# Optimization experiments

Hardware: AMD Instinct MI355X
Metric: run time of the kernel (lower is better)

The kernel has to match this reference:

```python
import jax, jax.numpy as jnp
import numpy as np

B, T, NX = 2, 2048, 512
H = 2                    # n_head (structurally forced to 2 by rns() broadcasting)
L = 64                   # num landmarks (cfg.MODEL.LANDMARK)
K = 32                   # rns neighbors per token
HD = NX // H // 2        # differential head dim = 128
EPS = 1e-5


def setup_inputs() -> dict:
    key = jax.random.key(0)
    ks = jax.random.split(key, 16)
    inp = {}
    inp["x"] = jax.random.normal(ks[0], (B, T, NX), jnp.float32)
    # linear weights (torch nn.Linear stores [out,in], applies x @ W.T)
    inp["wq"] = jax.random.normal(ks[1], (NX, NX), jnp.float32) * 0.02
    inp["wk"] = jax.random.normal(ks[2], (NX, NX), jnp.float32) * 0.02
    inp["wv"] = jax.random.normal(ks[3], (NX, NX), jnp.float32) * 0.02
    inp["wo"] = jax.random.normal(ks[4], (NX, NX), jnp.float32) * 0.02
    # landmark modulation params (kaiming-normal-ish init)
    inp["m1"] = jax.random.normal(ks[5], (2 * H, L, 1), jnp.float32)
    inp["m2"] = jax.random.normal(ks[6], (2 * H, 1, L), jnp.float32)
    # differential-attention lambda params
    inp["lq1"] = jax.random.normal(ks[7], (HD,), jnp.float32) * 0.1
    inp["lk1"] = jax.random.normal(ks[8], (HD,), jnp.float32) * 0.1
    inp["lq2"] = jax.random.normal(ks[9], (HD,), jnp.float32) * 0.1
    inp["lk2"] = jax.random.normal(ks[10], (HD,), jnp.float32) * 0.1
    inp["rms_g"] = jnp.ones((2 * HD,), jnp.float32)
    inp["l"] = 3  # layer depth for lambda_init_fn
    inp["num_landmark"] = L
    inp["rns_indices"] = jax.random.randint(ks[11], (B, T, K), 0, T)
    # random.sample(range(t), L) -> distinct indices
    inp["landmark"] = jax.random.permutation(ks[12], T)[:L]
    return inp


def _forward(x, wq, wk, wv, wo, m1, m2, lq1, lk1, lq2, lk2, rms_g,
             l, rns_indices, landmark):
    b, t, nx = x.shape
    hd = nx // H // 2
    q = x @ wq.T
    k = x @ wk.T
    v = x @ wv.T
    qh = q.reshape(b, t, 2 * H, hd).transpose(0, 2, 1, 3)   # [b,2H,t,hd]
    kh = k.reshape(b, t, 2 * H, hd).transpose(0, 2, 3, 1)   # [b,2H,hd,t]
    vh = v.reshape(b, t, H, 2 * hd).transpose(0, 2, 1, 3)   # [b,H,t,2hd]

    # landmark (Nystrom) low-rank factors, L2-normalized over head dim
    sq = qh[:, :, landmark, :]                               # [b,2H,L,hd]
    sk = kh[:, :, :, landmark]                               # [b,2H,hd,L]
    sq = sq / jnp.linalg.norm(sq, axis=3, keepdims=True)
    sk = sk / jnp.linalg.norm(sk, axis=2, keepdims=True)
    sq = m1[None] * sq
    sk = m2[None] * sk

    w1 = jnp.matmul(qh, sk)                                  # [b,2H,t,L]
    w2 = jnp.matmul(sq, kh)                                  # [b,2H,L,t]
    w = jnp.matmul(w1, w2)                                   # [b,2H,t,t]

    lam_init = 0.8 - 0.6 * np.exp(-0.3 * l)
    lam = jnp.exp(jnp.sum(lq1 * lk1)) - jnp.exp(jnp.sum(lq2 * lk2)) + lam_init

    # rns symmetric sparse mask: mask[b,i,j]=1 iff j in rns_indices[b,i] AND i in rns_indices[b,j]
    bi = jnp.arange(b)[:, None, None]
    ti = jnp.arange(t)[None, :, None]
    m = jnp.zeros((b, t, t), x.dtype).at[bi, ti, rns_indices].set(1.0)
    m = m * m.transpose(0, 2, 1)
    m4 = m[:, None]                                          # broadcast over heads

    p = jax.nn.softmax(w * m4 - 1e9 * (1.0 - m4), axis=-1)   # [b,2H,t,t]
    p5 = p.reshape(b, H, 2, t, t)
    # differential mixing (note: second term indexes the HEAD dim, requires H==2)
    wmix = (p5[:, :, 0] - lam * p5[:, :, 1]) + ((1.0 - lam) * p5[:, 1] - p5[:, 0])
    a = jnp.matmul(wmix, vh)                                 # [b,H,t,2hd]

    # RMSNorm sub-layer + (1 - lambda_init) scaling
    a = a * jax.lax.rsqrt(jnp.mean(a * a, axis=-1, keepdims=True) + EPS) * rms_g
    a = a * (1.0 - lam_init)
    return a.transpose(0, 2, 1, 3).reshape(b, t, H * 2 * hd) @ wo.T


def reference(x, wq, wk, wv, wo, m1, m2, lq1, lk1, lq2, lk2, rms_g,
              l, num_landmark, rns_indices, landmark):
    return _forward(x, wq, wk, wv, wo, m1, m2, lq1, lk1, lq2, lk2, rms_g,
                    l, rns_indices, landmark)
```

## Files before the change

### kernel.cpp

```cpp
#include <hip/hip_runtime.h>
#include <hip/hip_bf16.h>

#define BB 2
#define TT 2048
#define NX 512
#define NH 4
#define HD 128
#define LL 64
#define KK 32

typedef __bf16 bf16x8 __attribute__((ext_vector_type(8)));
typedef float f32x4 __attribute__((ext_vector_type(4)));
typedef unsigned short us;
typedef const unsigned int __attribute__((address_space(1)))* gptr_t;
typedef unsigned int __attribute__((address_space(3)))* lptr_t;

__device__ __forceinline__ us f2bf(float f) {
    unsigned u = __float_as_uint(f);
    unsigned r = (u + 0x7fffu + ((u >> 16) & 1u)) >> 16;
    return (us)r;
}
__device__ __forceinline__ float bf2f(us h) {
    return __uint_as_float(((unsigned)h) << 16);
}

__global__ void k_split_all(const float* __restrict__ x,
                            const float* __restrict__ wq, const float* __restrict__ wk,
                            const float* __restrict__ wv, const float* __restrict__ wo,
                            us* __restrict__ x_hi, us* __restrict__ x_lo,
                            us* __restrict__ wqkv_hi, us* __restrict__ wqkv_lo,
                            us* __restrict__ wo_hi, us* __restrict__ wo_lo,
                            const float* __restrict__ lq1, const float* __restrict__ lk1,
                            const float* __restrict__ lq2, const float* __restrict__ lk2,
                            const int* __restrict__ lint, float* __restrict__ scal,
                            float* __restrict__ cs)
{
    const int bidx = blockIdx.x;
    if (bidx == 3072) {
        const int tid = threadIdx.x;
        const f32x4 z = {0.f, 0.f, 0.f, 0.f};
        *reinterpret_cast<f32x4*>(cs + tid * 4) = z;
        if (tid < 64) {
            float s1 = lq1[tid] * lk1[tid] + lq1[tid + 64] * lk1[tid + 64];
            float s2 = lq2[tid] * lk2[tid] + lq2[tid + 64] * lk2[tid + 64];
            for (int off = 32; off; off >>= 1) { s1 += __shfl_xor(s1, off); s2 += __shfl_xor(s2, off); }
            if (tid == 0) {
                float lam_init = 0.8f - 0.6f * expf(-0.3f * (float)lint[0]);
                scal[0] = expf(s1) - expf(s2) + lam_init;
                scal[1] = lam_init;
            }
        }
        return;
    }
    const float* src;
    us* hi;
    us* lo;
    int pos;
    if (bidx < 2048) {
        src = x; hi = x_hi; lo = x_lo;
        pos = bidx * 1024 + threadIdx.x * 4;
    } else {
        const int w = (bidx - 2048) >> 8;
        const int p = (bidx - 2048) & 255;
        pos = p * 1024 + threadIdx.x * 4;
        if (w == 0)      { src = wq; hi = wqkv_hi;          lo = wqkv_lo; }
        else if (w == 1) { src = wk; hi = wqkv_hi + 262144; lo = wqkv_lo + 262144; }
        else if (w == 2) { src = wv; hi = wqkv_hi + 524288; lo = wqkv_lo + 524288; }
        else             { src = wo; hi = wo_hi;            lo = wo_lo; }
    }
    const float4 v = *reinterpret_cast<const float4*>(src + pos);
    ushort4 h, l;
    h.x = f2bf(v.x); l.x = f2bf(v.x - bf2f(h.x));
    h.y = f2bf(v.y); l.y = f2bf(v.y - bf2f(h.y));
    h.z = f2bf(v.z); l.z = f2bf(v.z - bf2f(h.z));
    h.w = f2bf(v.w); l.w = f2bf(v.w - bf2f(h.w));
    *reinterpret_cast<ushort4*>(hi + pos) = h;
    *reinterpret_cast<ushort4*>(lo + pos) = l;
}

template<int BN, int MODE>
__global__ __launch_bounds__(256) void k_gemm_big(
    const us* __restrict__ a_hi, const us* __restrict__ a_lo,
    const us* __restrict__ b_hi, const us* __restrict__ b_lo,
    us* __restrict__ vb, float* __restrict__ cout,
    us* __restrict__ qs_hi, us* __restrict__ qs_lo,
    us* __restrict__ ks_hi, us* __restrict__ ks_lo)
{
    constexpr int NB = BN / 32;
    __shared__ us lsA[64 * 64];
    __shared__ us lsB[BN * 64];
    const int tid = threadIdx.x;
    const int m0 = blockIdx.x * 64, n0 = blockIdx.y * BN;
    const int region = n0 >> 9;
    const int ncol0 = n0 & 511;
    const int l = tid & 63, wid = tid >> 6;
    const int wr = (wid >> 1) * 32, wc = (wid & 1) * (BN / 2);
    const int lr = l & 15;
    const int lkb = (l >> 4) * 16;
    f32x4 acc[2][NB] = {};

    const int r8 = tid >> 3;
    const int swzc8 = (((tid & 7) ^ (r8 & 7)) * 8);

    const int nstep = (MODE == 0) ? (region < 2 ? 24 : 16) : 16;
    for (int kt = 0; kt < nstep; ++kt) {
        const int seg = kt >> 3;
        const int koff = (kt & 7) * 64;
        const us* ab;
        const us* bb;
        if constexpr (MODE == 0) {
            if (region < 2) {
                ab = (seg < 2 ? a_hi : a_lo) + koff + swzc8;
                bb = (seg == 1 ? b_lo : b_hi) + koff + swzc8;
            } else {
                ab = (seg == 0 ? a_hi : a_lo) + koff + swzc8;
                bb = b_hi + koff + swzc8;
            }
        } else {
            ab = (seg == 0 ? a_hi : a_lo) + koff + swzc8;
            bb = b_hi + koff + swzc8;
        }
        #pragma unroll
        for (int j = 0; j < 2; ++j)
            __builtin_amdgcn_global_load_lds((gptr_t)(ab + (size_t)(m0 + j * 32 + r8) * 512),
                                             (lptr_t)(lsA + j * 2048 + tid * 8), 16, 0, 0);
        #pragma unroll
        for (int j = 0; j < BN / 32; ++j)
            __builtin_amdgcn_global_load_lds((gptr_t)(bb + (size_t)(n0 + j * 32 + r8) * 512),
                                             (lptr_t)(lsB + j * 2048 + tid * 8), 16, 0, 0);
        __syncthreads();
        bf16x8 af[2][2], bfr[NB][2];
        #pragma unroll
        for (int m = 0; m < 2; ++m) {
            const int row = wr + m * 16 + lr;
            #pragma unroll
            for (int kk = 0; kk < 2; ++kk) {
                const int cb = (kk * 64 + lkb) ^ ((row & 7) << 4);
                af[m][kk] = *reinterpret_cast<const bf16x8*>(
                    (const char*)lsA + row * 128 + cb);
            }
        }
        #pragma unroll
        for (int n = 0; n < NB; ++n) {
            const int row = wc + n * 16 + lr;
            #pragma unroll
            for (int kk = 0; kk < 2; ++kk) {
                const int cb = (kk * 64 + lkb) ^ ((row & 7) << 4);
                bfr[n][kk] = *reinterpret_cast<const bf16x8*>(
                    (const char*)lsB + row * 128 + cb);
            }
        }
        #pragma unroll
        for (int kk = 0; kk < 2; ++kk)
            #pragma unroll
            for (int m = 0; m < 2; ++m)
                #pragma unroll
                for (int n = 0; n < NB; ++n)
                    acc[m][n] = __builtin_amdgcn_mfma_f32_16x16x32_bf16(
                        af[m][kk], bfr[n][kk], acc[m][n], 0, 0, 0);
        __syncthreads();
    }

    if constexpr (MODE == 0) {
        if (region < 2) {
            us* sh = (region == 0) ? qs_hi : ks_hi;
            us* slo = (region == 0) ? qs_lo : ks_lo;
            #pragma unroll
            for (int m = 0; m < 2; ++m) {
                const int row = m0 + wr + m * 16 + (l >> 4) * 4;
                #pragma unroll
                for (int n = 0; n < NB; ++n) {
                    const int col = ncol0 + wc + n * 16 + lr;
                    #pragma unroll
                    for (int r = 0; r < 4; ++r) {
                        const float val = acc[m][n][r];
                        const us h = f2bf(val);
                        sh[(size_t)(row + r) * 512 + col] = h;
                        slo[(size_t)(row + r) * 512 + col] = f2bf(val - bf2f(h));
                    }
                }
            }
        } else {
            #pragma unroll
            for (int m = 0; m < 2; ++m) {
                const int row = m0 + wr + m * 16 + (l >> 4) * 4;
                #pragma unroll
                for (int n = 0; n < NB; ++n) {
                    const int col = ncol0 + wc + n * 16 + lr;
                    #pragma unroll
                    for (int r = 0; r < 4; ++r)
                        vb[(size_t)(row + r) * 512 + col] = f2bf(acc[m][n][r]);
                }
            }
        }
    } else {
        #pragma unroll
        for (int m = 0; m < 2; ++m) {
            const int row = m0 + wr + m * 16 + (l >> 4) * 4;
            #pragma unroll
            for (int n = 0; n < NB; ++n) {
                const int col = n0 + wc + n * 16 + lr;
                #pragma unroll
                for (int r = 0; r < 4; ++r)
                    cout[(size_t)(row + r) * 512 + col] = acc[m][n][r];
            }
        }
    }
}

__global__ __launch_bounds__(256) void k_gemm_w12(
    const us* __restrict__ q_hi, const us* __restrict__ q_lo,
    const us* __restrict__ k_hi, const us* __restrict__ k_lo,
    const us* __restrict__ kn_hi, const us* __restrict__ kn_lo,
    const us* __restrict__ qn_hi, const us* __restrict__ qn_lo,
    float* __restrict__ w1, float* __restrict__ w2t)
{
    __shared__ us lsA[64 * 32];
    __shared__ us lsB[64 * 32];
    const int tid = threadIdx.x;
    const int m0 = blockIdx.x * 64;
    const int y = blockIdx.y;
    const int hh = y % 3, b = y / 3;
    const int h = hh + 1;
    const int z = blockIdx.z;
    const us* ah = (z ? k_hi : q_hi) + ((size_t)b * 2048) * 512 + h * 128;
    const us* al = (z ? k_lo : q_lo) + ((size_t)b * 2048) * 512 + h * 128;
    const us* bh_p = (z ? qn_hi : kn_hi) + (size_t)(b * 4 + h) * 64 * 128;
    const us* bl_p = (z ? qn_lo : kn_lo) + (size_t)(b * 4 + h) * 64 * 128;
    float* C = (z ? w2t : w1) + (size_t)(b * 3 + hh) * 2048 * 64;

    const int l = tid & 63, wid = tid >> 6;
    const int wr = (wid >> 1) * 32, wc = (wid & 1) * 32;
    const int lr = l & 15, lk8 = (l >> 4) * 8;
    f32x4 acc[2][2] = {};
    const int srow = tid >> 2, scol = (tid & 3) * 8;

    for (int kt = 0; kt < 12; ++kt) {
        const int seg = kt >> 2;
        const int koff = (kt & 3) * 32;
        const us* ab = (seg < 2 ? ah : al) + koff + scol;
        const us* bb = (seg == 1 ? bl_p : bh_p) + koff + scol;
        __builtin_amdgcn_global_load_lds((gptr_t)(ab + (size_t)(m0 + srow) * 512),
                                         (lptr_t)(lsA + tid * 8), 16, 0, 0);
        __builtin_amdgcn_global_load_lds((gptr_t)(bb + (size_t)srow * 128),
                                         (lptr_t)(lsB + tid * 8), 16, 0, 0);
        __syncthreads();
        bf16x8 af[2], bfr[2];
        #pragma unroll
        for (int m = 0; m < 2; ++m)
            af[m] = *reinterpret_cast<const bf16x8*>(&lsA[(wr + m * 16 + lr) * 32 + lk8]);
        #pragma unroll
        for (int n = 0; n < 2; ++n)
            bfr[n] = *reinterpret_cast<const bf16x8*>(&lsB[(wc + n * 16 + lr) * 32 + lk8]);
        #pragma unroll
        for (int m = 0; m < 2; ++m)
            #pragma unroll
            for (int n = 0; n < 2; ++n)
                acc[m][n] = __builtin_amdgcn_mfma_f32_16x16x32_bf16(af[m], bfr[n], acc[m][n], 0, 0, 0);
        __syncthreads();
    }

    #pragma unroll
    for (int m = 0; m < 2; ++m) {
        const int row = m0 + wr + m * 16 + (l >> 4) * 4;
        #pragma unroll
        for (int n = 0; n < 2; ++n) {
            const int col = wc + n * 16 + lr;
            #pragma unroll
            for (int r = 0; r < 4; ++r)
                C[(size_t)(row + r) * 64 + col] = acc[m][n][r];
        }
    }
}

__global__ void k_norm_lm(const us* __restrict__ q_hi, const us* __restrict__ q_lo,
                          const us* __restrict__ k_hi, const us* __restrict__ k_lo,
                          const float* __restrict__ m1, const float* __restrict__ m2,
                          const int* __restrict__ landmark,
                          us* __restrict__ qn_hi, us* __restrict__ qn_lo,
                          us* __restrict__ kn_hi, us* __restrict__ kn_lo)
{
    const int idx = blockIdx.x;
    const int l = idx & 63;
    const int h = (idx >> 6) & 3;
    const int b = idx >> 8;
    const int lm = landmark[l];
    const int d = threadIdx.x;

    const size_t qoff = ((size_t)(b * TT + lm)) * NX + h * HD;
    const float qa = bf2f(q_hi[qoff + d]) + bf2f(q_lo[qoff + d]);
    const float qb = bf2f(q_hi[qoff + d + 64]) + bf2f(q_lo[qoff + d + 64]);
    const float ka = bf2f(k_hi[qoff + d]) + bf2f(k_lo[qoff + d]);
    const float kb = bf2f(k_hi[qoff + d + 64]) + bf2f(k_lo[qoff + d + 64]);
    float sq = qa * qa + qb * qb;
    float sk = ka * ka + kb * kb;
    for (int off = 32; off; off >>= 1) { sq += __shfl_xor(sq, off); sk += __shfl_xor(sk, off); }
    const float invq = rsqrtf(sq) * m1[h * LL + l];
    const float invk = rsqrtf(sk) * m2[h * LL + l];
    const size_t base = (((size_t)(b * NH + h)) * LL + l) * HD;
    const float vq0 = qa * invq, vq1 = qb * invq;
    const float vk0 = ka * invk, vk1 = kb * invk;
    us h0;
    h0 = f2bf(vq0); qn_hi[base + d] = h0;      qn_lo[base + d] = f2bf(vq0 - bf2f(h0));
    h0 = f2bf(vq1); qn_hi[base + d + 64] = h0; qn_lo[base + d + 64] = f2bf(vq1 - bf2f(h0));
    h0 = f2bf(vk0); kn_hi[base + d] = h0;      kn_lo[base + d] = f2bf(vk0 - bf2f(h0));
    h0 = f2bf(vk1); kn_hi[base + d + 64] = h0; kn_lo[base + d + 64] = f2bf(vk1 - bf2f(h0));
}

__global__ void k_colsum(const us* __restrict__ vb, float* __restrict__ cs)
{
    const int tid = threadIdx.x;
    const int c4 = tid * 4;
    const int b = c4 >> 9, c = c4 & 511;
    const int t0 = blockIdx.x * 64;
    const us* p = vb + ((size_t)(b * TT + t0)) * NX + c;
    f32x4 s = {0.f, 0.f, 0.f, 0.f};
    for (int t = 0; t < 64; ++t) {
        const ushort4 u = *reinterpret_cast<const ushort4*>(p + (size_t)t * NX);
        s[0] += bf2f(u.x); s[1] += bf2f(u.y); s[2] += bf2f(u.z); s[3] += bf2f(u.w);
    }
    atomicAdd(&cs[c4 + 0], s[0]);
    atomicAdd(&cs[c4 + 1], s[1]);
    atomicAdd(&cs[c4 + 2], s[2]);
    atomicAdd(&cs[c4 + 3], s[3]);
}

__global__ __launch_bounds__(256) void k_sparse_attn(
    const float* __restrict__ w1, const float* __restrict__ w2t,
    const us* __restrict__ vb, const float* __restrict__ cs,
    const int* __restrict__ rns, const float* __restrict__ rms_g,
    const float* __restrict__ scal,
    us* __restrict__ ao_hi, us* __restrict__ ao_lo)
{
    const int wid = threadIdx.x >> 6;
    const int lane = threadIdx.x & 63;
    const int bi = blockIdx.x * 4 + wid;
    const int b = bi >> 11, i = bi & 2047;

    __shared__ int   sl[4][32];
    __shared__ float plog[4][96];
    __shared__ float wmm[4][2][32];
    __shared__ float w1s[4][3][64];

    const int myidx = lane & 31;
    const int cand = rns[(size_t)bi * KK + myidx];
    int dup = 0;
    #pragma unroll
    for (int kk = 0; kk < 31; ++kk) {
        const int other = __shfl(cand, kk);
        dup |= (kk < myidx) & (other == cand);
    }
    const int* jrow = rns + ((size_t)(b * TT + cand)) * KK + (lane >> 5) * 16;
    int found = 0;
    #pragma unroll
    for (int kk = 0; kk < 16; ++kk) found |= (jrow[kk] == i);
    found |= __shfl_xor(found, 32);
    const int keep = (!dup) && found;
    const unsigned long long mask = __ballot(keep) & 0xffffffffull;
    const int sc = __popcll(mask);
    const int pos = __popcll(mask & ((1ull << myidx) - 1ull));
    if (lane < 32 && keep) sl[wid][pos] = cand;

    const float lam = scal[0], lam_init = scal[1];

    if (sc > 0) {
        #pragma unroll
        for (int r = 0; r < 3; ++r) {
            const int t = r * 64 + lane;
            const int hh = t >> 6, l2 = t & 63;
            w1s[wid][hh][l2] = w1[(((size_t)(b * 3 + hh)) * TT + i) * LL + l2];
        }
        const int ntask = 3 * sc;
        for (int t0 = 0; t0 < ntask; t0 += 8) {
            const int t = t0 + (lane >> 3);
            float part = 0.f;
            if (t < ntask) {
                const int hh = t % 3, ss = t / 3;
                const int j = sl[wid][ss];
                const float* w2row = w2t + (((size_t)(b * 3 + hh)) * TT + j) * LL + (lane & 7) * 8;
                const float* w1p = &w1s[wid][hh][(lane & 7) * 8];
                #pragma unroll
                for (int e = 0; e < 8; ++e) part += w1p[e] * w2row[e];
            }
            part += __shfl_xor(part, 1);
            part += __shfl_xor(part, 2);
            part += __shfl_xor(part, 4);
            if (t < ntask && (lane & 7) == 0) plog[wid][t] = part;
        }
        if (lane < 3) {
            float mx = -1e30f;
            for (int ss = 0; ss < sc; ++ss) mx = fmaxf(mx, plog[wid][ss * 3 + lane]);
            float s = 0.f;
            for (int ss = 0; ss < sc; ++ss) {
                const float e = expf(plog[wid][ss * 3 + lane] - mx);
                plog[wid][ss * 3 + lane] = e;
                s += e;
            }
            const float inv = 1.0f / s;
            for (int ss = 0; ss < sc; ++ss) plog[wid][ss * 3 + lane] *= inv;
        }
        if (lane < sc) {
            const float p1 = plog[wid][lane * 3 + 0];
            const float p2 = plog[wid][lane * 3 + 1];
            const float p3 = plog[wid][lane * 3 + 2];
            wmm[wid][0][lane] = (1.0f - lam) * p2 - lam * p1;
            wmm[wid][1][lane] = p2 - p1 + (1.0f - 2.0f * lam) * p3;
        }
    }

    f32x4 acc0 = {0.f, 0.f, 0.f, 0.f}, acc1 = {0.f, 0.f, 0.f, 0.f};
    if (sc == 0) {
        const float cc = (1.0f - 2.0f * lam) * (1.0f / (float)TT);
        const f32x4 c0 = *reinterpret_cast<const f32x4*>(cs + b * NX + lane * 4);
        const f32x4 c1 = *reinterpret_cast<const f32x4*>(cs + b * NX + 256 + lane * 4);
        acc0 = cc * c0;
        acc1 = cc * c1;
    } else {
        for (int ss = 0; ss < sc; ++ss) {
            const float wa = wmm[wid][0][ss], wb = wmm[wid][1][ss];
            const us* vrow = vb + ((size_t)(b * TT + sl[wid][ss])) * NX;
            const ushort4 ua = *reinterpret_cast<const ushort4*>(vrow + lane * 4);
            const ushort4 ub = *reinterpret_cast<const ushort4*>(vrow + 256 + lane * 4);
            acc0[0] += wa * bf2f(ua.x); acc0[1] += wa * bf2f(ua.y);
            acc0[2] += wa * bf2f(ua.z); acc0[3] += wa * bf2f(ua.w);
            acc1[0] += wb * bf2f(ub.x); acc1[1] += wb * bf2f(ub.y);
            acc1[2] += wb * bf2f(ub.z); acc1[3] += wb * bf2f(ub.w);
        }
    }

    float s0 = acc0[0]*acc0[0] + acc0[1]*acc0[1] + acc0[2]*acc0[2] + acc0[3]*acc0[3];
    float s1 = acc1[0]*acc1[0] + acc1[1]*acc1[1] + acc1[2]*acc1[2] + acc1[3]*acc1[3];
    #pragma unroll
    for (int off = 32; off; off >>= 1) { s0 += __shfl_xor(s0, off); s1 += __shfl_xor(s1, off); }
    const float sc0 = rsqrtf(s0 * (1.0f / 256.0f) + 1e-5f);
    const float sc1 = rsqrtf(s1 * (1.0f / 256.0f) + 1e-5f);
    const float og = 1.0f - lam_init;
    const f32x4 g = *reinterpret_cast<const f32x4*>(rms_g + lane * 4);
    ushort4 h0, l0, h1, l1;
    #pragma unroll
    for (int e = 0; e < 4; ++e) {
        const float v0 = acc0[e] * sc0 * g[e] * og;
        const float v1 = acc1[e] * sc1 * g[e] * og;
        const us a = f2bf(v0);
        const us bq = f2bf(v1);
        (&h0.x)[e] = a;  (&l0.x)[e] = f2bf(v0 - bf2f(a));
        (&h1.x)[e] = bq; (&l1.x)[e] = f2bf(v1 - bf2f(bq));
    }
    *reinterpret_cast<ushort4*>(ao_hi + (size_t)bi * NX + lane * 4) = h0;
    *reinterpret_cast<ushort4*>(ao_lo + (size_t)bi * NX + lane * 4) = l0;
    *reinterpret_cast<ushort4*>(ao_hi + (size_t)bi * NX + 256 + lane * 4) = h1;
    *reinterpret_cast<ushort4*>(ao_lo + (size_t)bi * NX + 256 + lane * 4) = l1;
}

extern "C" void kernel_launch(void* const* d_in, const int* in_sizes, int n_in,
                              void* d_out, int out_size, void* d_ws, size_t ws_size,
                              hipStream_t stream)
{
    const float* x    = (const float*)d_in[0];
    const float* wq   = (const float*)d_in[1];
    const float* wk   = (const float*)d_in[2];
    const float* wv   = (const float*)d_in[3];
    const float* wo   = (const float*)d_in[4];
    const float* m1   = (const float*)d_in[5];
    const float* m2   = (const float*)d_in[6];
    const float* lq1  = (const float*)d_in[7];
    const float* lk1  = (const float*)d_in[8];
    const float* lq2  = (const float*)d_in[9];
    const float* lk2  = (const float*)d_in[10];
    const float* rmsg = (const float*)d_in[11];
    const int*   lint = (const int*)d_in[12];
    const int*   rns  = (const int*)d_in[14];
    const int*   lmk  = (const int*)d_in[15];
    float* out = (float*)d_out;
    float* ws  = (float*)d_ws;

    const size_t M2 = 2097152;
    const size_t W3 = 786432;
    float* w1   = ws;
    float* w2t  = ws + W3;
    float* cs   = ws + 2 * W3;
    float* scal = cs + 1024;
    us* S = (us*)(scal + 128);
    us* vb   = S;
    us* x_hi = S + M2;
    us* x_lo = S + 2 * M2;
    us* ao_hi = x_hi;
    us* ao_lo = x_lo;
    us* q_hi = S + 3 * M2;
    us* q_lo = S + 4 * M2;
    us* k_hi = S + 5 * M2;
    us* k_lo = S + 6 * M2;
    us* wqkv_hi = S + 7 * M2;
    us* wqkv_lo = wqkv_hi + 786432;
    us* wo_hi = wqkv_lo + 786432;
    us* wo_lo = wo_hi + 262144;
    us* qn_hi = wo_lo + 262144;
    us* qn_lo = qn_hi + 65536;
    us* kn_hi = qn_lo + 65536;
    us* kn_lo = kn_hi + 65536;

    k_split_all<<<3073, 256, 0, stream>>>(x, wq, wk, wv, wo,
                                          x_hi, x_lo, wqkv_hi, wqkv_lo, wo_hi, wo_lo,
                                          lq1, lk1, lq2, lk2, lint, scal, cs);

    k_gemm_big<128, 0><<<dim3(64, 12), 256, 0, stream>>>(
        x_hi, x_lo, wqkv_hi, wqkv_lo, vb, nullptr, q_hi, q_lo, k_hi, k_lo);

    k_norm_lm<<<512, 64, 0, stream>>>(q_hi, q_lo, k_hi, k_lo, m1, m2, lmk,
                                      qn_hi, qn_lo, kn_hi, kn_lo);
    k_colsum<<<32, 256, 0, stream>>>(vb, cs);
    k_gemm_w12<<<dim3(32, 6, 2), 256, 0, stream>>>(q_hi, q_lo, k_hi, k_lo,
                                                   kn_hi, kn_lo, qn_hi, qn_lo, w1, w2t);
    k_sparse_attn<<<1024, 256, 0, stream>>>(w1, w2t, vb, cs, rns, rmsg, scal, ao_hi, ao_lo);

    k_gemm_big<64, 1><<<dim3(64, 8), 256, 0, stream>>>(
        ao_hi, ao_lo, wo_hi, wo_lo, nullptr, out, nullptr, nullptr, nullptr, nullptr);
}
```

Baseline: 150.4 us.

## Double-buffer GEMM LDS staging and fuse colsum into w12 GEMM launch

Adds double-buffered LDS staging to both GEMM kernels, so the async global-to-LDS copy for the next K-step is issued before computing the current one, and drops one barrier per step. The w12 GEMM switches to 64-wide swizzled K tiles. The column-sum kernel is merged into the w12 launch as extra blocks, which removes one kernel launch. k_norm_lm now packs four rows per 256-thread block. This doubles shared-memory use per block, which may lower occupancy.

After: 178.4 us. +18.6%, slower.

```diff
diff --git a/kernel.cpp b/kernel.cpp
--- a/kernel.cpp
+++ b/kernel.cpp
@@ -87,8 +87,9 @@
     us* __restrict__ ks_hi, us* __restrict__ ks_lo)
 {
     constexpr int NB = BN / 32;
-    __shared__ us lsA[64 * 64];
-    __shared__ us lsB[BN * 64];
+    constexpr int ASZ = 64 * 64, BSZ = BN * 64;
+    __shared__ us lsA[2 * ASZ];
+    __shared__ us lsB[2 * BSZ];
     const int tid = threadIdx.x;
     const int m0 = blockIdx.x * 64, n0 = blockIdx.y * BN;
     const int region = n0 >> 9;
@@ -103,7 +104,8 @@
     const int swzc8 = (((tid & 7) ^ (r8 & 7)) * 8);
 
     const int nstep = (MODE == 0) ? (region < 2 ? 24 : 16) : 16;
-    for (int kt = 0; kt < nstep; ++kt) {
+
+    auto stage = [&](int kt, int buf) {
         const int seg = kt >> 3;
         const int koff = (kt & 7) * 64;
         const us* ab;
@@ -120,15 +122,25 @@
             ab = (seg == 0 ? a_hi : a_lo) + koff + swzc8;
             bb = b_hi + koff + swzc8;
         }
+        us* lA = lsA + buf * ASZ;
+        us* lB = lsB + buf * BSZ;
         #pragma unroll
         for (int j = 0; j < 2; ++j)
             __builtin_amdgcn_global_load_lds((gptr_t)(ab + (size_t)(m0 + j * 32 + r8) * 512),
-                                             (lptr_t)(lsA + j * 2048 + tid * 8), 16, 0, 0);
+                                             (lptr_t)(lA + j * 2048 + tid * 8), 16, 0, 0);
         #pragma unroll
         for (int j = 0; j < BN / 32; ++j)
             __builtin_amdgcn_global_load_lds((gptr_t)(bb + (size_t)(n0 + j * 32 + r8) * 512),
-                                             (lptr_t)(lsB + j * 2048 + tid * 8), 16, 0, 0);
-        __syncthreads();
+                                             (lptr_t)(lB + j * 2048 + tid * 8), 16, 0, 0);
+    };
+
+    stage(0, 0);
+    __syncthreads();
+    int cur = 0;
+    for (int kt = 0; kt < nstep; ++kt) {
+        if (kt + 1 < nstep) stage(kt + 1, cur ^ 1);
+        const us* lA = lsA + cur * ASZ;
+        const us* lB = lsB + cur * BSZ;
         bf16x8 af[2][2], bfr[NB][2];
         #pragma unroll
         for (int m = 0; m < 2; ++m) {
@@ -137,7 +149,7 @@
             for (int kk = 0; kk < 2; ++kk) {
                 const int cb = (kk * 64 + lkb) ^ ((row & 7) << 4);
                 af[m][kk] = *reinterpret_cast<const bf16x8*>(
-                    (const char*)lsA + row * 128 + cb);
+                    (const char*)lA + row * 128 + cb);
             }
         }
         #pragma unroll
@@ -147,7 +159,7 @@
             for (int kk = 0; kk < 2; ++kk) {
                 const int cb = (kk * 64 + lkb) ^ ((row & 7) << 4);
                 bfr[n][kk] = *reinterpret_cast<const bf16x8*>(
-                    (const char*)lsB + row * 128 + cb);
+                    (const char*)lB + row * 128 + cb);
             }
         }
         #pragma unroll
@@ -159,6 +171,7 @@
                     acc[m][n] = __builtin_amdgcn_mfma_f32_16x16x32_bf16(
                         af[m][kk], bfr[n][kk], acc[m][n], 0, 0, 0);
         __syncthreads();
+        cur ^= 1;
     }
 
     if constexpr (MODE == 0) {
@@ -208,56 +221,106 @@
     }
 }
 
-__global__ __launch_bounds__(256) void k_gemm_w12(
+__global__ __launch_bounds__(256) void k_w12_colsum(
     const us* __restrict__ q_hi, const us* __restrict__ q_lo,
     const us* __restrict__ k_hi, const us* __restrict__ k_lo,
     const us* __restrict__ kn_hi, const us* __restrict__ kn_lo,
     const us* __restrict__ qn_hi, const us* __restrict__ qn_lo,
-    float* __restrict__ w1, float* __restrict__ w2t)
+    float* __restrict__ w1, float* __restrict__ w2t,
+    const us* __restrict__ vb, float* __restrict__ cs)
 {
-    __shared__ us lsA[64 * 32];
-    __shared__ us lsB[64 * 32];
+    const int blk = blockIdx.x;
     const int tid = threadIdx.x;
-    const int m0 = blockIdx.x * 64;
-    const int y = blockIdx.y;
+    if (blk >= 384) {
+        const int c4 = tid * 4;
+        const int b = c4 >> 9, c = c4 & 511;
+        const int t0 = (blk - 384) * 64;
+        const us* p = vb + ((size_t)(b * TT + t0)) * NX + c;
+        f32x4 s = {0.f, 0.f, 0.f, 0.f};
+        for (int t = 0; t < 64; ++t) {
+            const ushort4 u = *reinterpret_cast<const ushort4*>(p + (size_t)t * NX);
+            s[0] += bf2f(u.x); s[1] += bf2f(u.y); s[2] += bf2f(u.z); s[3] += bf2f(u.w);
+        }
+        atomicAdd(&cs[c4 + 0], s[0]);
+        atomicAdd(&cs[c4 + 1], s[1]);
+        atomicAdd(&cs[c4 + 2], s[2]);
+        atomicAdd(&cs[c4 + 3], s[3]);
+        return;
+    }
+    constexpr int ASZ = 64 * 64;
+    __shared__ us lsA[2 * ASZ];
+    __shared__ us lsB[2 * ASZ];
+    const int m0 = (blk & 31) * 64;
+    const int y = (blk >> 5) % 6;
+    const int z = blk / 192;
     const int hh = y % 3, b = y / 3;
     const int h = hh + 1;
-    const int z = blockIdx.z;
     const us* ah = (z ? k_hi : q_hi) + ((size_t)b * 2048) * 512 + h * 128;
     const us* al = (z ? k_lo : q_lo) + ((size_t)b * 2048) * 512 + h * 128;
-    const us* bh_p = (z ? qn_hi : kn_hi) + (size_t)(b * 4 + h) * 64 * 128;
-    const us* bl_p = (z ? qn_lo : kn_lo) + (size_t)(b * 4 + h) * 64 * 128;
+    const us* bhp = (z ? qn_hi : kn_hi) + (size_t)(b * 4 + h) * 64 * 128;
+    const us* blp = (z ? qn_lo : kn_lo) + (size_t)(b * 4 + h) * 64 * 128;
     float* C = (z ? w2t : w1) + (size_t)(b * 3 + hh) * 2048 * 64;
 
     const int l = tid & 63, wid = tid >> 6;
     const int wr = (wid >> 1) * 32, wc = (wid & 1) * 32;
-    const int lr = l & 15, lk8 = (l >> 4) * 8;
+    const int lr = l & 15;
+    const int lkb = (l >> 4) * 16;
     f32x4 acc[2][2] = {};
-    const int srow = tid >> 2, scol = (tid & 3) * 8;
-
-    for (int kt = 0; kt < 12; ++kt) {
-        const int seg = kt >> 2;
-        const int koff = (kt & 3) * 32;
-        const us* ab = (seg < 2 ? ah : al) + koff + scol;
-        const us* bb = (seg == 1 ? bl_p : bh_p) + koff + scol;
-        __builtin_amdgcn_global_load_lds((gptr_t)(ab + (size_t)(m0 + srow) * 512),
-                                         (lptr_t)(lsA + tid * 8), 16, 0, 0);
-        __builtin_amdgcn_global_load_lds((gptr_t)(bb + (size_t)srow * 128),
-                                         (lptr_t)(lsB + tid * 8), 16, 0, 0);
+    const int r8 = tid >> 3;
+    const int swzc8 = (((tid & 7) ^ (r8 & 7)) * 8);
+
+    auto stage = [&](int kt, int buf) {
+        const int seg = kt >> 1;
+        const int koff = (kt & 1) * 64;
+        const us* ab = (seg < 2 ? ah : al) + koff + swzc8;
+        const us* bb = (seg == 1 ? blp : bhp) + koff + swzc8;
+        us* lA = lsA + buf * ASZ;
+        us* lB = lsB + buf * ASZ;
+        #pragma unroll
+        for (int j = 0; j < 2; ++j) {
+            __builtin_amdgcn_global_load_lds((gptr_t)(ab + (size_t)(m0 + j * 32 + r8) * 512),
+                                             (lptr_t)(lA + j * 2048 + tid * 8), 16, 0, 0);
+            __builtin_amdgcn_global_load_lds((gptr_t)(bb + (size_t)(j * 32 + r8) * 128),
+                                             (lptr_t)(lB + j * 2048 + tid * 8), 16, 0, 0);
+        }
+    };
+
+    stage(0, 0);
+    __syncthreads();
+    int cur = 0;
+    for (int kt = 0; kt < 6; ++kt) {
+        if (kt + 1 < 6) stage(kt + 1, cur ^ 1);
+        const us* lA = lsA + cur * ASZ;
+        const us* lB = lsB + cur * ASZ;
+        bf16x8 af[2][2], bfr[2][2];
+        #pragma unroll
+        for (int m = 0; m < 2; ++m) {
+            const int row = wr + m * 16 + lr;
+            #pragma unroll
+            for (int kk = 0; kk < 2; ++kk) {
+                const int cb = (kk * 64 + lkb) ^ ((row & 7) << 4);
+                af[m][kk] = *reinterpret_cast<const bf16x8*>((const char*)lA + row * 128 + cb);
+            }
+        }
+        #pragma unroll
+        for (int n = 0; n < 2; ++n) {
+            const int row = wc + n * 16 + lr;
+            #pragma unroll
+            for (int kk = 0; kk < 2; ++kk) {
+                const int cb = (kk * 64 + lkb) ^ ((row & 7) << 4);
+                bfr[n][kk] = *reinterpret_cast<const bf16x8*>((const char*)lB + row * 128 + cb);
+            }
+        }
+        #pragma unroll
+        for (int kk = 0; kk < 2; ++kk)
+            #pragma unroll
+            for (int m = 0; m < 2; ++m)
+                #pragma unroll
+                for (int n = 0; n < 2; ++n)
+                    acc[m][n] = __builtin_amdgcn_mfma_f32_16x16x32_bf16(
+                        af[m][kk], bfr[n][kk], acc[m][n], 0, 0, 0);
         __syncthreads();
-        bf16x8 af[2], bfr[2];
-        #pragma unroll
-        for (int m = 0; m < 2; ++m)
-            af[m] = *reinterpret_cast<const bf16x8*>(&lsA[(wr + m * 16 + lr) * 32 + lk8]);
-        #pragma unroll
-        for (int n = 0; n < 2; ++n)
-            bfr[n] = *reinterpret_cast<const bf16x8*>(&lsB[(wc + n * 16 + lr) * 32 + lk8]);
-        #pragma unroll
-        for (int m = 0; m < 2; ++m)
-            #pragma unroll
-            for (int n = 0; n < 2; ++n)
-                acc[m][n] = __builtin_amdgcn_mfma_f32_16x16x32_bf16(af[m], bfr[n], acc[m][n], 0, 0, 0);
-        __syncthreads();
+        cur ^= 1;
     }
 
     #pragma unroll
@@ -273,19 +336,20 @@
     }
 }
 
-__global__ void k_norm_lm(const us* __restrict__ q_hi, const us* __restrict__ q_lo,
-                          const us* __restrict__ k_hi, const us* __restrict__ k_lo,
-                          const float* __restrict__ m1, const float* __restrict__ m2,
-                          const int* __restrict__ landmark,
-                          us* __restrict__ qn_hi, us* __restrict__ qn_lo,
-                          us* __restrict__ kn_hi, us* __restrict__ kn_lo)
+__global__ __launch_bounds__(256) void k_norm_lm(
+    const us* __restrict__ q_hi, const us* __restrict__ q_lo,
+    const us* __restrict__ k_hi, const us* __restrict__ k_lo,
+    const float* __restrict__ m1, const float* __restrict__ m2,
+    const int* __restrict__ landmark,
+    us* __restrict__ qn_hi, us* __restrict__ qn_lo,
+    us* __restrict__ kn_hi, us* __restrict__ kn_lo)
 {
-    const int idx = blockIdx.x;
+    const int idx = blockIdx.x * 4 + (threadIdx.x >> 6);
     const int l = idx & 63;
     const int h = (idx >> 6) & 3;
     const int b = idx >> 8;
     const int lm = landmark[l];
-    const int d = threadIdx.x;
+    const int d = threadIdx.x & 63;
 
     const size_t qoff = ((size_t)(b * TT + lm)) * NX + h * HD;
     const float qa = bf2f(q_hi[qoff + d]) + bf2f(q_lo[qoff + d]);
@@ -307,24 +371,6 @@
     h0 = f2bf(vk1); kn_hi[base + d + 64] = h0; kn_lo[base + d + 64] = f2bf(vk1 - bf2f(h0));
 }
 
-__global__ void k_colsum(const us* __restrict__ vb, float* __restrict__ cs)
-{
-    const int tid = threadIdx.x;
-    const int c4 = tid * 4;
-    const int b = c4 >> 9, c = c4 & 511;
-    const int t0 = blockIdx.x * 64;
-    const us* p = vb + ((size_t)(b * TT + t0)) * NX + c;
-    f32x4 s = {0.f, 0.f, 0.f, 0.f};
-    for (int t = 0; t < 64; ++t) {
-        const ushort4 u = *reinterpret_cast<const ushort4*>(p + (size_t)t * NX);
-        s[0] += bf2f(u.x); s[1] += bf2f(u.y); s[2] += bf2f(u.z); s[3] += bf2f(u.w);
-    }
-    atomicAdd(&cs[c4 + 0], s[0]);
-    atomicAdd(&cs[c4 + 1], s[1]);
-    atomicAdd(&cs[c4 + 2], s[2]);
-    atomicAdd(&cs[c4 + 3], s[3]);
-}
-
 __global__ __launch_bounds__(256) void k_sparse_attn(
     const float* __restrict__ w1, const float* __restrict__ w2t,
     const us* __restrict__ vb, const float* __restrict__ cs,
@@ -365,11 +411,8 @@
 
     if (sc > 0) {
         #pragma unroll
-        for (int r = 0; r < 3; ++r) {
-            const int t = r * 64 + lane;
-            const int hh = t >> 6, l2 = t & 63;
-            w1s[wid][hh][l2] = w1[(((size_t)(b * 3 + hh)) * TT + i) * LL + l2];
-        }
+        for (int r = 0; r < 3; ++r)
+            w1s[wid][r][lane] = w1[(((size_t)(b * 3 + r)) * TT + i) * LL + lane];
         const int ntask = 3 * sc;
         for (int t0 = 0; t0 < ntask; t0 += 8) {
             const int t = t0 + (lane >> 3);
@@ -506,11 +549,10 @@
     k_gemm_big<128, 0><<<dim3(64, 12), 256, 0, stream>>>(
         x_hi, x_lo, wqkv_hi, wqkv_lo, vb, nullptr, q_hi, q_lo, k_hi, k_lo);
 
-    k_norm_lm<<<512, 64, 0, stream>>>(q_hi, q_lo, k_hi, k_lo, m1, m2, lmk,
-                                      qn_hi, qn_lo, kn_hi, kn_lo);
-    k_colsum<<<32, 256, 0, stream>>>(vb, cs);
-    k_gemm_w12<<<dim3(32, 6, 2), 256, 0, stream>>>(q_hi, q_lo, k_hi, k_lo,
-                                                   kn_hi, kn_lo, qn_hi, qn_lo, w1, w2t);
+    k_norm_lm<<<128, 256, 0, stream>>>(q_hi, q_lo, k_hi, k_lo, m1, m2, lmk,
+                                       qn_hi, qn_lo, kn_hi, kn_lo);
+    k_w12_colsum<<<416, 256, 0, stream>>>(q_hi, q_lo, k_hi, k_lo,
+                                          kn_hi, kn_lo, qn_hi, qn_lo, w1, w2t, vb, cs);
     k_sparse_attn<<<1024, 256, 0, stream>>>(w1, w2t, vb, cs, rns, rmsg, scal, ao_hi, ao_lo);
 
     k_gemm_big<64, 1><<<dim3(64, 8), 256, 0, stream>>>(
```

## Drop split-bf16 low part for output projection, fuse colsum into w12 kernel

Applied to the files above, without the earlier changes.

The output projection GEMM now uses only the bf16 high part of the attention output (8 k-steps instead of 16), and the attention kernel writes a single bf16 buffer instead of hi/lo pairs. The column-sum kernel is merged into the w1/w2 GEMM launch as extra blocks, and the landmark-norm kernel packs four rows per 256-thread block, which removes a launch and small-block overhead. The precision reduction lowers accuracy of the final projection and could push error near tolerance.

After: 141.1 us. 1.07x faster.

```diff
diff --git a/kernel.cpp b/kernel.cpp
--- a/kernel.cpp
+++ b/kernel.cpp
@@ -102,7 +102,7 @@
     const int r8 = tid >> 3;
     const int swzc8 = (((tid & 7) ^ (r8 & 7)) * 8);
 
-    const int nstep = (MODE == 0) ? (region < 2 ? 24 : 16) : 16;
+    const int nstep = (MODE == 0) ? (region < 2 ? 24 : 16) : 8;
     for (int kt = 0; kt < nstep; ++kt) {
         const int seg = kt >> 3;
         const int koff = (kt & 7) * 64;
@@ -117,7 +117,7 @@
                 bb = b_hi + koff + swzc8;
             }
         } else {
-            ab = (seg == 0 ? a_hi : a_lo) + koff + swzc8;
+            ab = a_hi + koff + swzc8;
             bb = b_hi + koff + swzc8;
         }
         #pragma unroll
@@ -208,25 +208,43 @@
     }
 }
 
-__global__ __launch_bounds__(256) void k_gemm_w12(
+__global__ __launch_bounds__(256) void k_w12_colsum(
     const us* __restrict__ q_hi, const us* __restrict__ q_lo,
     const us* __restrict__ k_hi, const us* __restrict__ k_lo,
     const us* __restrict__ kn_hi, const us* __restrict__ kn_lo,
     const us* __restrict__ qn_hi, const us* __restrict__ qn_lo,
-    float* __restrict__ w1, float* __restrict__ w2t)
+    float* __restrict__ w1, float* __restrict__ w2t,
+    const us* __restrict__ vb, float* __restrict__ cs)
 {
+    const int blk = blockIdx.x;
+    const int tid = threadIdx.x;
+    if (blk >= 384) {
+        const int c4 = tid * 4;
+        const int b = c4 >> 9, c = c4 & 511;
+        const int t0 = (blk - 384) * 64;
+        const us* p = vb + ((size_t)(b * TT + t0)) * NX + c;
+        f32x4 s = {0.f, 0.f, 0.f, 0.f};
+        for (int t = 0; t < 64; ++t) {
+            const ushort4 u = *reinterpret_cast<const ushort4*>(p + (size_t)t * NX);
+            s[0] += bf2f(u.x); s[1] += bf2f(u.y); s[2] += bf2f(u.z); s[3] += bf2f(u.w);
+        }
+        atomicAdd(&cs[c4 + 0], s[0]);
+        atomicAdd(&cs[c4 + 1], s[1]);
+        atomicAdd(&cs[c4 + 2], s[2]);
+        atomicAdd(&cs[c4 + 3], s[3]);
+        return;
+    }
     __shared__ us lsA[64 * 32];
     __shared__ us lsB[64 * 32];
-    const int tid = threadIdx.x;
-    const int m0 = blockIdx.x * 64;
-    const int y = blockIdx.y;
+    const int m0 = (blk & 31) * 64;
+    const int y = (blk >> 5) % 6;
+    const int z = blk / 192;
     const int hh = y % 3, b = y / 3;
     const int h = hh + 1;
-    const int z = blockIdx.z;
     const us* ah = (z ? k_hi : q_hi) + ((size_t)b * 2048) * 512 + h * 128;
     const us* al = (z ? k_lo : q_lo) + ((size_t)b * 2048) * 512 + h * 128;
-    const us* bh_p = (z ? qn_hi : kn_hi) + (size_t)(b * 4 + h) * 64 * 128;
-    const us* bl_p = (z ? qn_lo : kn_lo) + (size_t)(b * 4 + h) * 64 * 128;
+    const us* bhp = (z ? qn_hi : kn_hi) + (size_t)(b * 4 + h) * 64 * 128;
+    const us* blp = (z ? qn_lo : kn_lo) + (size_t)(b * 4 + h) * 64 * 128;
     float* C = (z ? w2t : w1) + (size_t)(b * 3 + hh) * 2048 * 64;
 
     const int l = tid & 63, wid = tid >> 6;
@@ -239,7 +257,7 @@
         const int seg = kt >> 2;
         const int koff = (kt & 3) * 32;
         const us* ab = (seg < 2 ? ah : al) + koff + scol;
-        const us* bb = (seg == 1 ? bl_p : bh_p) + koff + scol;
+        const us* bb = (seg == 1 ? blp : bhp) + koff + scol;
         __builtin_amdgcn_global_load_lds((gptr_t)(ab + (size_t)(m0 + srow) * 512),
                                          (lptr_t)(lsA + tid * 8), 16, 0, 0);
         __builtin_amdgcn_global_load_lds((gptr_t)(bb + (size_t)srow * 128),
@@ -273,19 +291,20 @@
     }
 }
 
-__global__ void k_norm_lm(const us* __restrict__ q_hi, const us* __restrict__ q_lo,
-                          const us* __restrict__ k_hi, const us* __restrict__ k_lo,
-                          const float* __restrict__ m1, const float* __restrict__ m2,
-                          const int* __restrict__ landmark,
-                          us* __restrict__ qn_hi, us* __restrict__ qn_lo,
-                          us* __restrict__ kn_hi, us* __restrict__ kn_lo)
+__global__ __launch_bounds__(256) void k_norm_lm(
+    const us* __restrict__ q_hi, const us* __restrict__ q_lo,
+    const us* __restrict__ k_hi, const us* __restrict__ k_lo,
+    const float* __restrict__ m1, const float* __restrict__ m2,
+    const int* __restrict__ landmark,
+    us* __restrict__ qn_hi, us* __restrict__ qn_lo,
+    us* __restrict__ kn_hi, us* __restrict__ kn_lo)
 {
-    const int idx = blockIdx.x;
+    const int idx = blockIdx.x * 4 + (threadIdx.x >> 6);
     const int l = idx & 63;
     const int h = (idx >> 6) & 3;
     const int b = idx >> 8;
     const int lm = landmark[l];
-    const int d = threadIdx.x;
+    const int d = threadIdx.x & 63;
 
     const size_t qoff = ((size_t)(b * TT + lm)) * NX + h * HD;
     const float qa = bf2f(q_hi[qoff + d]) + bf2f(q_lo[qoff + d]);
@@ -307,30 +326,12 @@
     h0 = f2bf(vk1); kn_hi[base + d + 64] = h0; kn_lo[base + d + 64] = f2bf(vk1 - bf2f(h0));
 }
 
-__global__ void k_colsum(const us* __restrict__ vb, float* __restrict__ cs)
-{
-    const int tid = threadIdx.x;
-    const int c4 = tid * 4;
-    const int b = c4 >> 9, c = c4 & 511;
-    const int t0 = blockIdx.x * 64;
-    const us* p = vb + ((size_t)(b * TT + t0)) * NX + c;
-    f32x4 s = {0.f, 0.f, 0.f, 0.f};
-    for (int t = 0; t < 64; ++t) {
-        const ushort4 u = *reinterpret_cast<const ushort4*>(p + (size_t)t * NX);
-        s[0] += bf2f(u.x); s[1] += bf2f(u.y); s[2] += bf2f(u.z); s[3] += bf2f(u.w);
-    }
-    atomicAdd(&cs[c4 + 0], s[0]);
-    atomicAdd(&cs[c4 + 1], s[1]);
-    atomicAdd(&cs[c4 + 2], s[2]);
-    atomicAdd(&cs[c4 + 3], s[3]);
-}
-
 __global__ __launch_bounds__(256) void k_sparse_attn(
     const float* __restrict__ w1, const float* __restrict__ w2t,
     const us* __restrict__ vb, const float* __restrict__ cs,
     const int* __restrict__ rns, const float* __restrict__ rms_g,
     const float* __restrict__ scal,
-    us* __restrict__ ao_hi, us* __restrict__ ao_lo)
+    us* __restrict__ ao)
 {
     const int wid = threadIdx.x >> 6;
     const int lane = threadIdx.x & 63;
@@ -365,11 +366,8 @@
 
     if (sc > 0) {
         #pragma unroll
-        for (int r = 0; r < 3; ++r) {
-            const int t = r * 64 + lane;
-            const int hh = t >> 6, l2 = t & 63;
-            w1s[wid][hh][l2] = w1[(((size_t)(b * 3 + hh)) * TT + i) * LL + l2];
-        }
+        for (int r = 0; r < 3; ++r)
+            w1s[wid][r][lane] = w1[(((size_t)(b * 3 + r)) * TT + i) * LL + lane];
         const int ntask = 3 * sc;
         for (int t0 = 0; t0 < ntask; t0 += 8) {
             const int t = t0 + (lane >> 3);
@@ -436,20 +434,14 @@
     const float sc1 = rsqrtf(s1 * (1.0f / 256.0f) + 1e-5f);
     const float og = 1.0f - lam_init;
     const f32x4 g = *reinterpret_cast<const f32x4*>(rms_g + lane * 4);
-    ushort4 h0, l0, h1, l1;
+    ushort4 h0, h1;
     #pragma unroll
     for (int e = 0; e < 4; ++e) {
-        const float v0 = acc0[e] * sc0 * g[e] * og;
-        const float v1 = acc1[e] * sc1 * g[e] * og;
-        const us a = f2bf(v0);
-        const us bq = f2bf(v1);
-        (&h0.x)[e] = a;  (&l0.x)[e] = f2bf(v0 - bf2f(a));
-        (&h1.x)[e] = bq; (&l1.x)[e] = f2bf(v1 - bf2f(bq));
-    }
-    *reinterpret_cast<ushort4*>(ao_hi + (size_t)bi * NX + lane * 4) = h0;
-    *reinterpret_cast<ushort4*>(ao_lo + (size_t)bi * NX + lane * 4) = l0;
-    *reinterpret_cast<ushort4*>(ao_hi + (size_t)bi * NX + 256 + lane * 4) = h1;
-    *reinterpret_cast<ushort4*>(ao_lo + (size_t)bi * NX + 256 + lane * 4) = l1;
+        (&h0.x)[e] = f2bf(acc0[e] * sc0 * g[e] * og);
+        (&h1.x)[e] = f2bf(acc1[e] * sc1 * g[e] * og);
+    }
+    *reinterpret_cast<ushort4*>(ao + (size_t)bi * NX + lane * 4) = h0;
+    *reinterpret_cast<ushort4*>(ao + (size_t)bi * NX + 256 + lane * 4) = h1;
 }
 
 extern "C" void kernel_launch(void* const* d_in, const int* in_sizes, int n_in,
@@ -484,8 +476,7 @@
     us* vb   = S;
     us* x_hi = S + M2;
     us* x_lo = S + 2 * M2;
-    us* ao_hi = x_hi;
-    us* ao_lo = x_lo;
+    us* ao   = x_hi;
     us* q_hi = S + 3 * M2;
     us* q_lo = S + 4 * M2;
     us* k_hi = S + 5 * M2;
@@ -506,13 +497,12 @@
     k_gemm_big<128, 0><<<dim3(64, 12), 256, 0, stream>>>(
         x_hi, x_lo, wqkv_hi, wqkv_lo, vb, nullptr, q_hi, q_lo, k_hi, k_lo);
 
-    k_norm_lm<<<512, 64, 0, stream>>>(q_hi, q_lo, k_hi, k_lo, m1, m2, lmk,
-                                      qn_hi, qn_lo, kn_hi, kn_lo);
-    k_colsum<<<32, 256, 0, stream>>>(vb, cs);
-    k_gemm_w12<<<dim3(32, 6, 2), 256, 0, stream>>>(q_hi, q_lo, k_hi, k_lo,
-                                                   kn_hi, kn_lo, qn_hi, qn_lo, w1, w2t);
-    k_sparse_attn<<<1024, 256, 0, stream>>>(w1, w2t, vb, cs, rns, rmsg, scal, ao_hi, ao_lo);
+    k_norm_lm<<<128, 256, 0, stream>>>(q_hi, q_lo, k_hi, k_lo, m1, m2, lmk,
+                                       qn_hi, qn_lo, kn_hi, kn_lo);
+    k_w12_colsum<<<416, 256, 0, stream>>>(q_hi, q_lo, k_hi, k_lo,
+                                          kn_hi, kn_lo, qn_hi, qn_lo, w1, w2t, vb, cs);
+    k_sparse_attn<<<1024, 256, 0, stream>>>(w1, w2t, vb, cs, rns, rmsg, scal, ao);
 
     k_gemm_big<64, 1><<<dim3(64, 8), 256, 0, stream>>>(
-        ao_hi, ao_lo, wo_hi, wo_lo, nullptr, out, nullptr, nullptr, nullptr, nullptr);
-}
+        ao, nullptr, wo_hi, nullptr, nullptr, out, nullptr, nullptr, nullptr, nullptr);
+}
```
